# Performance work log

Measured on AMD Instinct MI355X. Metric: run time of the kernel, lower is better.

The kernel has to match this reference:

```python
import jax, jax.numpy as jnp
import numpy as np

LN_EPS = 1e-5  # torch nn.LayerNorm default


def setup_inputs() -> dict:
    key = jax.random.key(0)
    kx, kw = jax.random.split(key)
    tokens, d_in, d_out = 8192, 4096, 16384
    x = jax.random.normal(kx, (tokens, d_in), dtype=jnp.float32)
    # nn.Linear weight layout: [out_features, in_features]
    W = jax.random.normal(kw, (d_out, d_in), dtype=jnp.float32) * (1.0 / np.sqrt(d_in))
    return {"x": x, "W": W}


def reference(x, W):
    # LayerNorm over last dim, no affine params (elementwise_affine=False)
    mean = jnp.mean(x, axis=-1, keepdims=True)
    var = jnp.mean(jnp.square(x - mean), axis=-1, keepdims=True)  # biased, as torch LN
    xn = (x - mean) * jax.lax.rsqrt(var + LN_EPS)
    # Linear (no bias): [tokens, d_in] @ [d_in, d_out]
    y = jnp.einsum("td,od->to", xn, W)
    return jax.nn.sigmoid(y)
```

## Files before the change

kernel.cpp:

```cpp
#include <hip/hip_runtime.h>
#include <hip/hip_bf16.h>
#include <stdint.h>

#define TOKENS 8192
#define DIN    4096
#define DOUT   16384

#define BM 256
#define BN 256
#define BKT 64
#define NT (DIN / BKT)
#define NJ (NT / 2)

typedef short s16x8 __attribute__((ext_vector_type(8)));
typedef float f32x4 __attribute__((ext_vector_type(4)));

#define AS1 __attribute__((address_space(1)))
#define AS3 __attribute__((address_space(3)))
#define VMCNT(n)  asm volatile("s_waitcnt vmcnt(" #n ")" ::: "memory")
#define BAR()     __builtin_amdgcn_s_barrier()

__device__ __forceinline__ unsigned short f2bf(float f) {
  unsigned int u = __float_as_uint(f);
  u += 0x7fffu + ((u >> 16) & 1u);
  return (unsigned short)(u >> 16);
}

__global__ __launch_bounds__(256) void ln_kernel(const float* __restrict__ x,
                                                 unsigned short* __restrict__ xn) {
  const int row = blockIdx.x;
  const float4* xr = reinterpret_cast<const float4*>(x + (size_t)row * DIN);
  float4 v[4];
  float sum = 0.f, ssq = 0.f;
#pragma unroll
  for (int i = 0; i < 4; ++i) {
    v[i] = xr[threadIdx.x + i * 256];
    sum += v[i].x + v[i].y + v[i].z + v[i].w;
    ssq += v[i].x * v[i].x + v[i].y * v[i].y + v[i].z * v[i].z + v[i].w * v[i].w;
  }
#pragma unroll
  for (int off = 32; off > 0; off >>= 1) {
    sum += __shfl_xor(sum, off, 64);
    ssq += __shfl_xor(ssq, off, 64);
  }
  __shared__ float red[8];
  const int wid = threadIdx.x >> 6;
  if ((threadIdx.x & 63) == 0) { red[wid] = sum; red[wid + 4] = ssq; }
  __syncthreads();
  sum = red[0] + red[1] + red[2] + red[3];
  ssq = red[4] + red[5] + red[6] + red[7];
  const float mean = sum * (1.f / DIN);
  const float var  = ssq * (1.f / DIN) - mean * mean;
  const float rs   = rsqrtf(var + 1e-5f);
  ushort4* xo = reinterpret_cast<ushort4*>(xn + (size_t)row * DIN);
#pragma unroll
  for (int i = 0; i < 4; ++i) {
    ushort4 o;
    o.x = f2bf((v[i].x - mean) * rs);
    o.y = f2bf((v[i].y - mean) * rs);
    o.z = f2bf((v[i].z - mean) * rs);
    o.w = f2bf((v[i].w - mean) * rs);
    xo[threadIdx.x + i * 256] = o;
  }
}

__global__ __launch_bounds__(256) void cvt_kernel(const float* __restrict__ W,
                                                  unsigned short* __restrict__ Wb) {
  const size_t i = (size_t)blockIdx.x * 256 + threadIdx.x;
  float4 v = reinterpret_cast<const float4*>(W)[i];
  ushort4 o;
  o.x = f2bf(v.x); o.y = f2bf(v.y); o.z = f2bf(v.z); o.w = f2bf(v.w);
  reinterpret_cast<ushort4*>(Wb)[i] = o;
}

__global__ __launch_bounds__(512, 2) void gemm_sig(const unsigned short* __restrict__ A,
                                                   const unsigned short* __restrict__ B,
                                                   float* __restrict__ C) {
  __shared__ unsigned short Asl[2 * 256 * 64];
  __shared__ unsigned short Bsl[2 * 256 * 64];

  const int bid = blockIdx.x;
  const int cpx = gridDim.x >> 3;
  const int swz = (bid & 7) * cpx + (bid >> 3);
  const int bm = swz & 31;
  const int bn = swz >> 5;

  const int tid  = threadIdx.x;
  const int wid  = tid >> 6;
  const int lane = tid & 63;
  const int wr = wid >> 2, wc = wid & 3;

  const unsigned short* gA = A + (size_t)bm * BM * DIN;
  const unsigned short* gB = B + (size_t)bn * BN * DIN;

  const int l8 = lane >> 3, l7 = lane & 7;
  const int csw = l7 ^ l8;
  const unsigned short* sA = gA + (size_t)(wid * 8 + l8) * DIN + csw * 8;
  const unsigned short* sB = gB + (size_t)(wid * 8 + l8) * DIN + csw * 8;
  const int dOfs = wid * 512;

#define STG_Aq(p, q, kt) __builtin_amdgcn_global_load_lds( \
    (const AS1 void*)(sA + (size_t)(q) * 64 * DIN + (size_t)(kt) * BKT), \
    (AS3 void*)(Asl + ((p) * 256 + (q) * 64) * 64 + dOfs), 16, 0, 0)
#define STG_Bq(p, q, kt) __builtin_amdgcn_global_load_lds( \
    (const AS1 void*)(sB + (size_t)(q) * 64 * DIN + (size_t)(kt) * BKT), \
    (AS3 void*)(Bsl + ((p) * 256 + (q) * 64) * 64 + dOfs), 16, 0, 0)

  int aO[8], bO[4], slt[2];
#pragma unroll
  for (int m = 0; m < 8; ++m) aO[m] = (wr * 128 + m * 16 + (lane & 15)) * 64;
#pragma unroll
  for (int n = 0; n < 4; ++n) bO[n] = (wc * 64 + n * 16 + (lane & 15)) * 64;
  slt[0] = ((lane >> 4) ^ l7) * 8;
  slt[1] = (((lane >> 4) + 4) ^ l7) * 8;

  s16x8 afX[4], afY[4], bf0[4], bf1[4];
  f32x4 acc[8][4] = {};

#define RD_A(p, mb4, kh, dst) do { _Pragma("unroll") for (int mm = 0; mm < 4; ++mm) \
    dst[mm] = *reinterpret_cast<const s16x8*>(Asl + (p) * 16384 + aO[(mb4) + mm] + slt[kh]); } while (0)
#define RD_B(p, kh, dst) do { _Pragma("unroll") for (int nn = 0; nn < 4; ++nn) \
    dst[nn] = *reinterpret_cast<const s16x8*>(Bsl + (p) * 16384 + bO[nn] + slt[kh]); } while (0)
#define MM(mb4, afr, bfr) do { _Pragma("unroll") for (int mm = 0; mm < 4; ++mm) \
    _Pragma("unroll") for (int nn = 0; nn < 4; ++nn) \
      acc[(mb4) + mm][nn] = __builtin_amdgcn_mfma_f32_16x16x32_bf16(afr[mm], bfr[nn], acc[(mb4) + mm][nn], 0, 0, 0); } while (0)
#define PRIO1() __builtin_amdgcn_s_setprio(1)
#define PRIO0() __builtin_amdgcn_s_setprio(0)

  STG_Aq(0, 0, 0); STG_Aq(0, 1, 0); STG_Aq(0, 2, 0); STG_Aq(0, 3, 0);
  STG_Bq(0, 0, 0); STG_Bq(0, 1, 0); STG_Bq(0, 2, 0); STG_Bq(0, 3, 0);
  STG_Aq(1, 0, 1); STG_Aq(1, 2, 1);
  STG_Bq(1, 0, 1); STG_Bq(1, 1, 1); STG_Bq(1, 2, 1); STG_Bq(1, 3, 1);
  VMCNT(6); BAR();
  RD_A(0, 0, 0, afX); RD_B(0, 0, bf0);

  for (int j = 0; j < NJ - 1; ++j) {
    const int t1 = 2 * j + 1, t2 = 2 * j + 2, t3 = 2 * j + 3;
    VMCNT(8); RD_A(0, 0, 1, afY); RD_B(0, 1, bf1);
    STG_Aq(1, 1, t1); STG_Aq(1, 3, t1);
    BAR(); PRIO1(); MM(0, afX, bf0); PRIO0(); BAR();
    VMCNT(8); RD_A(0, 4, 0, afX);
    BAR(); PRIO1(); MM(0, afY, bf1); PRIO0(); BAR();
    VMCNT(8); RD_A(0, 4, 1, afY);
    STG_Bq(0, 0, t2); STG_Bq(0, 1, t2); STG_Bq(0, 2, t2); STG_Bq(0, 3, t2);
    STG_Aq(0, 0, t2); STG_Aq(0, 2, t2);
    BAR(); PRIO1(); MM(4, afX, bf0); PRIO0(); BAR();
    VMCNT(8); RD_A(1, 0, 0, afX); RD_B(1, 0, bf0);
    BAR(); PRIO1(); MM(4, afY, bf1); PRIO0(); BAR();
    VMCNT(8); RD_A(1, 0, 1, afY); RD_B(1, 1, bf1);
    STG_Aq(0, 1, t2); STG_Aq(0, 3, t2);
    BAR(); PRIO1(); MM(0, afX, bf0); PRIO0(); BAR();
    VMCNT(8); RD_A(1, 4, 0, afX);
    BAR(); PRIO1(); MM(0, afY, bf1); PRIO0(); BAR();
    VMCNT(8); RD_A(1, 4, 1, afY);
    STG_Bq(1, 0, t3); STG_Bq(1, 1, t3); STG_Bq(1, 2, t3); STG_Bq(1, 3, t3);
    STG_Aq(1, 0, t3); STG_Aq(1, 2, t3);
    BAR(); PRIO1(); MM(4, afX, bf0); PRIO0(); BAR();
    VMCNT(8); RD_A(0, 0, 0, afX); RD_B(0, 0, bf0);
    BAR(); PRIO1(); MM(4, afY, bf1); PRIO0(); BAR();
  }

  {
    const int t1 = NT - 1;
    VMCNT(8); RD_A(0, 0, 1, afY); RD_B(0, 1, bf1);
    STG_Aq(1, 1, t1); STG_Aq(1, 3, t1);
    BAR(); PRIO1(); MM(0, afX, bf0); PRIO0(); BAR();
    VMCNT(8); RD_A(0, 4, 0, afX);
    BAR(); PRIO1(); MM(0, afY, bf1); PRIO0(); BAR();
    VMCNT(8); RD_A(0, 4, 1, afY);
    BAR(); PRIO1(); MM(4, afX, bf0); PRIO0(); BAR();
    VMCNT(2); RD_A(1, 0, 0, afX); RD_B(1, 0, bf0);
    BAR(); PRIO1(); MM(4, afY, bf1); PRIO0(); BAR();
    VMCNT(2); RD_A(1, 0, 1, afY); RD_B(1, 1, bf1);
    BAR(); PRIO1(); MM(0, afX, bf0); PRIO0(); BAR();
    VMCNT(0); RD_A(1, 4, 0, afX);
    BAR(); PRIO1(); MM(0, afY, bf1); PRIO0(); BAR();
    VMCNT(0); RD_A(1, 4, 1, afY);
    BAR(); PRIO1(); MM(4, afX, bf0); PRIO0(); BAR();
    PRIO1(); MM(4, afY, bf1); PRIO0();
  }

#undef STG_Aq
#undef STG_Bq
#undef RD_A
#undef RD_B
#undef MM

  const int crow0 = bm * BM + wr * 128 + (lane >> 4) * 4;
  const int ccol0 = bn * BN + wc * 64 + (lane & 15);
#pragma unroll
  for (int m = 0; m < 8; ++m)
#pragma unroll
    for (int n = 0; n < 4; ++n)
#pragma unroll
      for (int jj = 0; jj < 4; ++jj) {
        const float v = acc[m][n][jj];
        C[(size_t)(crow0 + m * 16 + jj) * DOUT + (ccol0 + n * 16)] = 1.f / (1.f + __expf(-v));
      }
}

extern "C" void kernel_launch(void* const* d_in, const int* in_sizes, int n_in,
                              void* d_out, int out_size, void* d_ws, size_t ws_size,
                              hipStream_t stream) {
  const float* x = (const float*)d_in[0];
  const float* W = (const float*)d_in[1];
  float* out = (float*)d_out;

  unsigned short* xn = (unsigned short*)d_ws;
  unsigned short* Wb = xn + (size_t)TOKENS * DIN;

  ln_kernel<<<TOKENS, 256, 0, stream>>>(x, xn);
  cvt_kernel<<<((size_t)DOUT * DIN) / 1024, 256, 0, stream>>>(W, Wb);
  gemm_sig<<<(TOKENS / BM) * (DOUT / BN), 512, 0, stream>>>(xn, Wb, out);
}
```

Baseline: 1.283 ms.

## Switch GEMM to 32x32x16 MFMA with reworked LDS pipeline and tile swizzle

Replaces the 16x16x32 bf16 MFMA tiles with 32x32x16 MFMA, so each wave holds 4x2 accumulators of 16 floats and reads a full 64-wide K slice of A and B fragments per phase. The main loop is restructured into four compute phases per two K tiles, with a different interleaving of global-to-LDS loads and waits. The block index mapping is also changed to group tiles into 2x2 blocks for L2 reuse. The larger MFMA shape reduces LDS fragment reads per flop, at the cost of larger register fragments and a different store pattern in the sigmoid epilogue.

Result: faster. 1.119 ms (-12.8%).

```diff
diff --git a/kernel.cpp b/kernel.cpp
--- a/kernel.cpp
+++ b/kernel.cpp
@@ -13,12 +13,14 @@
 #define NJ (NT / 2)
 
 typedef short s16x8 __attribute__((ext_vector_type(8)));
-typedef float f32x4 __attribute__((ext_vector_type(4)));
+typedef float f32x16 __attribute__((ext_vector_type(16)));
 
 #define AS1 __attribute__((address_space(1)))
 #define AS3 __attribute__((address_space(3)))
 #define VMCNT(n)  asm volatile("s_waitcnt vmcnt(" #n ")" ::: "memory")
 #define BAR()     __builtin_amdgcn_s_barrier()
+#define PRIO1()   __builtin_amdgcn_s_setprio(1)
+#define PRIO0()   __builtin_amdgcn_s_setprio(0)
 
 __device__ __forceinline__ unsigned short f2bf(float f) {
   unsigned int u = __float_as_uint(f);
@@ -82,8 +84,10 @@
   const int bid = blockIdx.x;
   const int cpx = gridDim.x >> 3;
   const int swz = (bid & 7) * cpx + (bid >> 3);
-  const int bm = swz & 31;
-  const int bn = swz >> 5;
+  const int grp = swz >> 2;
+  const int sub = swz & 3;
+  const int bm = ((grp & 15) << 1) | (sub & 1);
+  const int bn = ((grp >> 4) << 1) | (sub >> 1);
 
   const int tid  = threadIdx.x;
   const int wid  = tid >> 6;
@@ -106,96 +110,87 @@
     (const AS1 void*)(sB + (size_t)(q) * 64 * DIN + (size_t)(kt) * BKT), \
     (AS3 void*)(Bsl + ((p) * 256 + (q) * 64) * 64 + dOfs), 16, 0, 0)
 
-  int aO[8], bO[4], slt[2];
-#pragma unroll
-  for (int m = 0; m < 8; ++m) aO[m] = (wr * 128 + m * 16 + (lane & 15)) * 64;
-#pragma unroll
-  for (int n = 0; n < 4; ++n) bO[n] = (wc * 64 + n * 16 + (lane & 15)) * 64;
-  slt[0] = ((lane >> 4) ^ l7) * 8;
-  slt[1] = (((lane >> 4) + 4) ^ l7) * 8;
-
-  s16x8 afX[4], afY[4], bf0[4], bf1[4];
-  f32x4 acc[8][4] = {};
-
-#define RD_A(p, mb4, kh, dst) do { _Pragma("unroll") for (int mm = 0; mm < 4; ++mm) \
-    dst[mm] = *reinterpret_cast<const s16x8*>(Asl + (p) * 16384 + aO[(mb4) + mm] + slt[kh]); } while (0)
-#define RD_B(p, kh, dst) do { _Pragma("unroll") for (int nn = 0; nn < 4; ++nn) \
-    dst[nn] = *reinterpret_cast<const s16x8*>(Bsl + (p) * 16384 + bO[nn] + slt[kh]); } while (0)
-#define MM(mb4, afr, bfr) do { _Pragma("unroll") for (int mm = 0; mm < 4; ++mm) \
-    _Pragma("unroll") for (int nn = 0; nn < 4; ++nn) \
-      acc[(mb4) + mm][nn] = __builtin_amdgcn_mfma_f32_16x16x32_bf16(afr[mm], bfr[nn], acc[(mb4) + mm][nn], 0, 0, 0); } while (0)
-#define PRIO1() __builtin_amdgcn_s_setprio(1)
-#define PRIO0() __builtin_amdgcn_s_setprio(0)
+  const int l31 = lane & 31;
+  const int l5  = lane >> 5;
+  int aRow[4], bRow[2], kslt[4];
+#pragma unroll
+  for (int mb = 0; mb < 4; ++mb) aRow[mb] = (wr * 128 + mb * 32 + l31) * 64;
+#pragma unroll
+  for (int nb = 0; nb < 2; ++nb) bRow[nb] = (wc * 64 + nb * 32 + l31) * 64;
+#pragma unroll
+  for (int ks = 0; ks < 4; ++ks) kslt[ks] = ((2 * ks + l5) ^ l7) * 8;
+
+  s16x8 a0[4], a1[4], b0[4], b1[4];
+  f32x16 acc[4][2] = {};
+
+#define RD_AP(p, mp) do { _Pragma("unroll") for (int ks = 0; ks < 4; ++ks) { \
+    a0[ks] = *reinterpret_cast<const s16x8*>(Asl + (p) * 16384 + aRow[2 * (mp)] + kslt[ks]); \
+    a1[ks] = *reinterpret_cast<const s16x8*>(Asl + (p) * 16384 + aRow[2 * (mp) + 1] + kslt[ks]); } } while (0)
+#define RD_BALL(p) do { _Pragma("unroll") for (int ks = 0; ks < 4; ++ks) { \
+    b0[ks] = *reinterpret_cast<const s16x8*>(Bsl + (p) * 16384 + bRow[0] + kslt[ks]); \
+    b1[ks] = *reinterpret_cast<const s16x8*>(Bsl + (p) * 16384 + bRow[1] + kslt[ks]); } } while (0)
+#define MMPH(mp) do { _Pragma("unroll") for (int ks = 0; ks < 4; ++ks) { \
+    acc[2 * (mp)][0]     = __builtin_amdgcn_mfma_f32_32x32x16_bf16(a0[ks], b0[ks], acc[2 * (mp)][0], 0, 0, 0); \
+    acc[2 * (mp)][1]     = __builtin_amdgcn_mfma_f32_32x32x16_bf16(a0[ks], b1[ks], acc[2 * (mp)][1], 0, 0, 0); \
+    acc[2 * (mp) + 1][0] = __builtin_amdgcn_mfma_f32_32x32x16_bf16(a1[ks], b0[ks], acc[2 * (mp) + 1][0], 0, 0, 0); \
+    acc[2 * (mp) + 1][1] = __builtin_amdgcn_mfma_f32_32x32x16_bf16(a1[ks], b1[ks], acc[2 * (mp) + 1][1], 0, 0, 0); } } while (0)
 
   STG_Aq(0, 0, 0); STG_Aq(0, 1, 0); STG_Aq(0, 2, 0); STG_Aq(0, 3, 0);
   STG_Bq(0, 0, 0); STG_Bq(0, 1, 0); STG_Bq(0, 2, 0); STG_Bq(0, 3, 0);
-  STG_Aq(1, 0, 1); STG_Aq(1, 2, 1);
   STG_Bq(1, 0, 1); STG_Bq(1, 1, 1); STG_Bq(1, 2, 1); STG_Bq(1, 3, 1);
-  VMCNT(6); BAR();
-  RD_A(0, 0, 0, afX); RD_B(0, 0, bf0);
+  VMCNT(4); BAR();
 
   for (int j = 0; j < NJ - 1; ++j) {
     const int t1 = 2 * j + 1, t2 = 2 * j + 2, t3 = 2 * j + 3;
-    VMCNT(8); RD_A(0, 0, 1, afY); RD_B(0, 1, bf1);
-    STG_Aq(1, 1, t1); STG_Aq(1, 3, t1);
-    BAR(); PRIO1(); MM(0, afX, bf0); PRIO0(); BAR();
-    VMCNT(8); RD_A(0, 4, 0, afX);
-    BAR(); PRIO1(); MM(0, afY, bf1); PRIO0(); BAR();
-    VMCNT(8); RD_A(0, 4, 1, afY);
-    STG_Bq(0, 0, t2); STG_Bq(0, 1, t2); STG_Bq(0, 2, t2); STG_Bq(0, 3, t2);
-    STG_Aq(0, 0, t2); STG_Aq(0, 2, t2);
-    BAR(); PRIO1(); MM(4, afX, bf0); PRIO0(); BAR();
-    VMCNT(8); RD_A(1, 0, 0, afX); RD_B(1, 0, bf0);
-    BAR(); PRIO1(); MM(4, afY, bf1); PRIO0(); BAR();
-    VMCNT(8); RD_A(1, 0, 1, afY); RD_B(1, 1, bf1);
-    STG_Aq(0, 1, t2); STG_Aq(0, 3, t2);
-    BAR(); PRIO1(); MM(0, afX, bf0); PRIO0(); BAR();
-    VMCNT(8); RD_A(1, 4, 0, afX);
-    BAR(); PRIO1(); MM(0, afY, bf1); PRIO0(); BAR();
-    VMCNT(8); RD_A(1, 4, 1, afY);
+    VMCNT(4);
+    RD_AP(0, 0); RD_BALL(0);
+    STG_Aq(1, 0, t1); STG_Aq(1, 1, t1); STG_Aq(1, 2, t1); STG_Aq(1, 3, t1);
+    BAR(); PRIO1(); MMPH(0); PRIO0(); BAR();
+    RD_AP(0, 1);
+    STG_Aq(0, 0, t2); STG_Aq(0, 2, t2); STG_Bq(0, 0, t2); STG_Bq(0, 1, t2);
+    BAR(); PRIO1(); MMPH(1); PRIO0(); BAR();
+    VMCNT(4);
+    RD_AP(1, 0); RD_BALL(1);
+    STG_Bq(0, 2, t2); STG_Bq(0, 3, t2); STG_Aq(0, 1, t2); STG_Aq(0, 3, t2);
+    BAR(); PRIO1(); MMPH(0); PRIO0(); BAR();
+    RD_AP(1, 1);
     STG_Bq(1, 0, t3); STG_Bq(1, 1, t3); STG_Bq(1, 2, t3); STG_Bq(1, 3, t3);
-    STG_Aq(1, 0, t3); STG_Aq(1, 2, t3);
-    BAR(); PRIO1(); MM(4, afX, bf0); PRIO0(); BAR();
-    VMCNT(8); RD_A(0, 0, 0, afX); RD_B(0, 0, bf0);
-    BAR(); PRIO1(); MM(4, afY, bf1); PRIO0(); BAR();
+    BAR(); PRIO1(); MMPH(1); PRIO0(); BAR();
   }
 
   {
     const int t1 = NT - 1;
-    VMCNT(8); RD_A(0, 0, 1, afY); RD_B(0, 1, bf1);
-    STG_Aq(1, 1, t1); STG_Aq(1, 3, t1);
-    BAR(); PRIO1(); MM(0, afX, bf0); PRIO0(); BAR();
-    VMCNT(8); RD_A(0, 4, 0, afX);
-    BAR(); PRIO1(); MM(0, afY, bf1); PRIO0(); BAR();
-    VMCNT(8); RD_A(0, 4, 1, afY);
-    BAR(); PRIO1(); MM(4, afX, bf0); PRIO0(); BAR();
-    VMCNT(2); RD_A(1, 0, 0, afX); RD_B(1, 0, bf0);
-    BAR(); PRIO1(); MM(4, afY, bf1); PRIO0(); BAR();
-    VMCNT(2); RD_A(1, 0, 1, afY); RD_B(1, 1, bf1);
-    BAR(); PRIO1(); MM(0, afX, bf0); PRIO0(); BAR();
-    VMCNT(0); RD_A(1, 4, 0, afX);
-    BAR(); PRIO1(); MM(0, afY, bf1); PRIO0(); BAR();
-    VMCNT(0); RD_A(1, 4, 1, afY);
-    BAR(); PRIO1(); MM(4, afX, bf0); PRIO0(); BAR();
-    PRIO1(); MM(4, afY, bf1); PRIO0();
+    VMCNT(4);
+    RD_AP(0, 0); RD_BALL(0);
+    STG_Aq(1, 0, t1); STG_Aq(1, 1, t1); STG_Aq(1, 2, t1); STG_Aq(1, 3, t1);
+    BAR(); PRIO1(); MMPH(0); PRIO0(); BAR();
+    RD_AP(0, 1);
+    BAR(); PRIO1(); MMPH(1); PRIO0(); BAR();
+    VMCNT(0);
+    RD_AP(1, 0); RD_BALL(1);
+    BAR(); PRIO1(); MMPH(0); PRIO0(); BAR();
+    RD_AP(1, 1);
+    BAR(); PRIO1(); MMPH(1); PRIO0(); BAR();
   }
 
 #undef STG_Aq
 #undef STG_Bq
-#undef RD_A
-#undef RD_B
-#undef MM
-
-  const int crow0 = bm * BM + wr * 128 + (lane >> 4) * 4;
-  const int ccol0 = bn * BN + wc * 64 + (lane & 15);
-#pragma unroll
-  for (int m = 0; m < 8; ++m)
-#pragma unroll
-    for (int n = 0; n < 4; ++n)
-#pragma unroll
-      for (int jj = 0; jj < 4; ++jj) {
-        const float v = acc[m][n][jj];
-        C[(size_t)(crow0 + m * 16 + jj) * DOUT + (ccol0 + n * 16)] = 1.f / (1.f + __expf(-v));
+#undef RD_AP
+#undef RD_BALL
+#undef MMPH
+
+  const int crow0 = bm * BM + wr * 128 + 4 * l5;
+  const int ccol0 = bn * BN + wc * 64 + l31;
+#pragma unroll
+  for (int mb = 0; mb < 4; ++mb)
+#pragma unroll
+    for (int nb = 0; nb < 2; ++nb)
+#pragma unroll
+      for (int reg = 0; reg < 16; ++reg) {
+        const int r = crow0 + mb * 32 + (reg & 3) + 8 * (reg >> 2);
+        const int c = ccol0 + nb * 32;
+        const float v = acc[mb][nb][reg];
+        C[(size_t)r * DOUT + c] = 1.f / (1.f + __expf(-v));
       }
 }
 
```
